# Kernel optimization log

Hardware: AMD Instinct MI355X
Metric: run time of the kernel (lower is better)

## Reference

```python
import jax, jax.numpy as jnp
import numpy as np

N, E, B = 25000, 400000, 64
IN, HID, OUT, EDGE, TDIM, L = 16, 128, 16, 16, 64, 4
EIN = 2 * HID + 1 + EDGE  # 273


def _sinusoidal(t, dim):
    half = dim // 2
    freqs = jnp.exp(jnp.arange(half, dtype=jnp.float32) * (-np.log(10000.0) / (half - 1)))
    a = t[:, None] * freqs[None, :]
    return jnp.concatenate([jnp.sin(a), jnp.cos(a)], axis=-1)


def _layernorm(h, g, b, eps=1e-5):
    mu = h.mean(-1, keepdims=True)
    v = h.var(-1, keepdims=True)
    return (h - mu) / jnp.sqrt(v + eps) * g + b


def setup_inputs() -> dict:
    key = jax.random.key(0)
    ks = iter(jax.random.split(key, 64))

    def rn(shape, scale=0.05):
        return jax.random.normal(next(ks), shape, dtype=jnp.float32) * scale

    inp = {
        'h': jax.random.normal(next(ks), (N, IN), dtype=jnp.float32),
        'x': jax.random.normal(next(ks), (N, 3), dtype=jnp.float32),
        'edge_index': jax.random.randint(next(ks), (2, E), 0, N),
        't': jax.random.uniform(next(ks), (B,), dtype=jnp.float32) * 1000.0,
        'edge_attr': jax.random.normal(next(ks), (E, EDGE), dtype=jnp.float32),
        'batch': jnp.sort(jax.random.randint(next(ks), (N,), 0, B)),
        # embeddings
        'node_w': rn((IN, HID)), 'node_b': jnp.zeros((HID,), jnp.float32),
        'tw1': rn((TDIM, HID)), 'tb1': jnp.zeros((HID,), jnp.float32),
        'tw2': rn((HID, HID)), 'tb2': jnp.zeros((HID,), jnp.float32),
        # per-layer stacked params (L, ...)
        'edge_w1': rn((L, EIN, HID)), 'edge_b1': jnp.zeros((L, HID), jnp.float32),
        'edge_w2': rn((L, HID, HID)), 'edge_b2': jnp.zeros((L, HID), jnp.float32),
        'att_w': rn((L, HID, 1)), 'att_b': jnp.zeros((L, 1), jnp.float32),
        'cw1': rn((L, HID, HID)), 'cb1': jnp.zeros((L, HID), jnp.float32),
        'cw2': rn((L, HID, 1), scale=0.001),  # xavier gain=0.001
        'nw1': rn((L, 2 * HID, HID)), 'nb1': jnp.zeros((L, HID), jnp.float32),
        'nw2': rn((L, HID, HID)), 'nb2': jnp.zeros((L, HID), jnp.float32),
        'ln_g': jnp.ones((L, HID), jnp.float32), 'ln_b': jnp.zeros((L, HID), jnp.float32),
        # heads
        'out_w1': rn((HID, HID)), 'out_b1': jnp.zeros((HID,), jnp.float32),
        'out_w2': rn((HID, OUT)), 'out_b2': jnp.zeros((OUT,), jnp.float32),
        'head_w': rn((HID, 3), scale=0.01), 'head_b': jnp.zeros((3,), jnp.float32),
    }
    return inp


def reference(h, x, edge_index, t, edge_attr, batch,
              node_w, node_b, tw1, tb1, tw2, tb2,
              edge_w1, edge_b1, edge_w2, edge_b2, att_w, att_b,
              cw1, cb1, cw2, nw1, nb1, nw2, nb2, ln_g, ln_b,
              out_w1, out_b1, out_w2, out_b2, head_w, head_b):
    silu = jax.nn.silu
    n_nodes = h.shape[0]
    row, col = edge_index[0], edge_index[1]

    # node + time embedding
    h = h @ node_w + node_b
    te = _sinusoidal(t, TDIM)
    te = silu(te @ tw1 + tb1) @ tw2 + tb2
    h = h + te[batch]

    for i in range(L):
        coord_diff = x[row] - x[col]                      # (E, 3)
        radial = (coord_diff ** 2).sum(-1, keepdims=True)  # (E, 1)
        edge_in = jnp.concatenate([h[row], h[col], radial, edge_attr], axis=-1)
        m = silu(silu(edge_in @ edge_w1[i] + edge_b1[i]) @ edge_w2[i] + edge_b2[i])
        att = jax.nn.sigmoid(m @ att_w[i] + att_b[i])
        m = m * att
        cw = silu(m @ cw1[i] + cb1[i]) @ cw2[i]           # (E, 1)
        coord_diff = coord_diff / jnp.sqrt(radial + 1e-8)  # normalize=True
        x = x + jax.ops.segment_sum(coord_diff * cw, row, num_segments=n_nodes)
        m_i = jax.ops.segment_sum(m, row, num_segments=n_nodes)
        h_in = jnp.concatenate([h, m_i], axis=-1)
        h_new = h + (silu(h_in @ nw1[i] + nb1[i]) @ nw2[i] + nb2[i])
        h = _layernorm(h_new, ln_g[i], ln_b[i])

    h_out = silu(h @ out_w1 + out_b1) @ out_w2 + out_b2  # (N, OUT)
    x_out = h @ head_w + head_b                           # (N, 3)
    return h_out, x_out
```

## Files before the change

### kernel.cpp

```cpp
#include <hip/hip_runtime.h>
#include <cmath>

#define NN      25000
#define NEDGE   400000
#define NBATCH  64
#define IN_DIM  16
#define HID     128
#define OUT_DIM 16
#define EDGE_DIM 16
#define TDIM    64
#define NL      4
#define EIN     273
#define EPB     64
#define W1KB    36
#define W2KB    16
#define A_PAD   65
#define A3OFF   (16*A_PAD*8)

typedef short bfrag __attribute__((ext_vector_type(8)));
typedef float ffrag __attribute__((ext_vector_type(4)));

__device__ __forceinline__ float siluf(float v) { return v / (1.f + __expf(-v)); }
__device__ __forceinline__ float sigm(float v)  { return 1.f / (1.f + __expf(-v)); }
__device__ __forceinline__ unsigned short f2b(float f) {
    unsigned u = __float_as_uint(f);
    u = (u + 0x7FFFu + ((u >> 16) & 1u)) >> 16;
    return (unsigned short)u;
}
__device__ __forceinline__ float b2f(unsigned short b) {
    return __uint_as_float(((unsigned)b) << 16);
}

__global__ __launch_bounds__(256) void hist_kernel(const int* __restrict__ row, int* __restrict__ deg) {
    const int tid = blockIdx.x * 256 + threadIdx.x;
    if (tid < NEDGE) atomicAdd(&deg[row[tid]], 1);
}

__global__ __launch_bounds__(1024) void scan_kernel(const int* __restrict__ deg, int* __restrict__ row_start) {
    __shared__ int part[1024];
    const int tid = threadIdx.x;
    const int base = tid * 25;
    int sum = 0;
    for (int i = 0; i < 25; i++) { const int idx = base + i; if (idx < NN) sum += deg[idx]; }
    part[tid] = sum;
    __syncthreads();
    for (int off = 1; off < 1024; off <<= 1) {
        int v = (tid >= off) ? part[tid - off] : 0;
        __syncthreads();
        part[tid] += v;
        __syncthreads();
    }
    int run = part[tid] - sum;
    for (int i = 0; i < 25; i++) {
        const int idx = base + i;
        if (idx < NN) { row_start[idx] = run; run += deg[idx]; }
    }
    if (tid == 1023) row_start[NN] = part[1023];
}

__global__ __launch_bounds__(256) void scatter_kernel(
    const int* __restrict__ row, const int* __restrict__ col,
    const int* __restrict__ row_start, int* __restrict__ cursor,
    int* __restrict__ rowp, int* __restrict__ colp, int* __restrict__ eorder)
{
    const int tid = blockIdx.x * 256 + threadIdx.x;
    if (tid >= NEDGE) return;
    const int r = row[tid];
    const int pos = row_start[r] + atomicAdd(&cursor[r], 1);
    rowp[pos] = r; colp[pos] = col[tid]; eorder[pos] = tid;
}

__global__ __launch_bounds__(256) void ea_pack(
    const float* __restrict__ ea, const int* __restrict__ eorder, unsigned short* __restrict__ eabp)
{
    const int tid = blockIdx.x * 256 + threadIdx.x;
    if (tid >= NEDGE) return;
    const int e = eorder[tid];
    const float4* src = (const float4*)&ea[(size_t)e * 16];
    bfrag o0, o1;
    #pragma unroll
    for (int q = 0; q < 2; q++) {
        const float4 a = src[q];
        o0[q*4+0] = (short)f2b(a.x); o0[q*4+1] = (short)f2b(a.y);
        o0[q*4+2] = (short)f2b(a.z); o0[q*4+3] = (short)f2b(a.w);
    }
    #pragma unroll
    for (int q = 0; q < 2; q++) {
        const float4 a = src[2+q];
        o1[q*4+0] = (short)f2b(a.x); o1[q*4+1] = (short)f2b(a.y);
        o1[q*4+2] = (short)f2b(a.z); o1[q*4+3] = (short)f2b(a.w);
    }
    *(bfrag*)&eabp[(size_t)tid * 16]     = o0;
    *(bfrag*)&eabp[(size_t)tid * 16 + 8] = o1;
}

__global__ __launch_bounds__(256) void prep_w(
    const float* __restrict__ ew1, const float* __restrict__ ew2, const float* __restrict__ cw1,
    unsigned short* __restrict__ w1p, unsigned short* __restrict__ w2p, unsigned short* __restrict__ c1p)
{
    const int PER_L = 68 * 128;
    int tid = blockIdx.x * 256 + threadIdx.x;
    if (tid >= NL * PER_L) return;
    const int l = tid / PER_L, rem = tid % PER_L;
    const int kb = rem >> 7, n = rem & 127;
    unsigned short o[8];
    if (kb < W1KB) {
        const float* W = ew1 + (size_t)l * EIN * HID;
        #pragma unroll
        for (int j = 0; j < 8; j++) {
            const int k = kb * 8 + j;
            const int ok = (k < 256) ? k : (k < 272 ? k + 1 : (k == 272 ? 256 : -1));
            o[j] = (ok >= 0) ? f2b(W[(size_t)ok * HID + n]) : (unsigned short)0;
        }
        #pragma unroll
        for (int j = 0; j < 8; j++) w1p[(((size_t)l * W1KB + kb) * 128 + n) * 8 + j] = o[j];
    } else if (kb < W1KB + W2KB) {
        const int kb2 = kb - W1KB;
        const float* W = ew2 + (size_t)l * HID * HID;
        #pragma unroll
        for (int j = 0; j < 8; j++) o[j] = f2b(W[(size_t)(kb2 * 8 + j) * HID + n]);
        #pragma unroll
        for (int j = 0; j < 8; j++) w2p[(((size_t)l * W2KB + kb2) * 128 + n) * 8 + j] = o[j];
    } else {
        const int kb2 = kb - W1KB - W2KB;
        const float* W = cw1 + (size_t)l * HID * HID;
        #pragma unroll
        for (int j = 0; j < 8; j++) o[j] = f2b(W[(size_t)(kb2 * 8 + j) * HID + n]);
        #pragma unroll
        for (int j = 0; j < 8; j++) c1p[(((size_t)l * W2KB + kb2) * 128 + n) * 8 + j] = o[j];
    }
}

__global__ __launch_bounds__(256) void prep_w2(
    const float* __restrict__ nw1, const float* __restrict__ nw2,
    const float* __restrict__ ow1, const float* __restrict__ ow2,
    unsigned short* __restrict__ n1p, unsigned short* __restrict__ n2p,
    unsigned short* __restrict__ o1p, unsigned short* __restrict__ o2p)
{
    const int C1 = NL * 32 * 128;
    const int C2 = C1 + NL * 16 * 128;
    const int C3 = C2 + 16 * 128;
    const int C4 = C3 + 16 * 16;
    int tid = blockIdx.x * 256 + threadIdx.x;
    if (tid >= C4) return;
    if (tid < C1) {
        const int l = tid / (32*128), rem = tid % (32*128);
        const int kb = rem >> 7, n = rem & 127;
        #pragma unroll
        for (int j = 0; j < 8; j++)
            n1p[(size_t)tid*8 + j] = f2b(nw1[((size_t)l*256 + kb*8 + j)*128 + n]);
    } else if (tid < C2) {
        const int t2 = tid - C1;
        const int l = t2 / (16*128), rem = t2 % (16*128);
        const int kb = rem >> 7, n = rem & 127;
        #pragma unroll
        for (int j = 0; j < 8; j++)
            n2p[(size_t)t2*8 + j] = f2b(nw2[((size_t)l*128 + kb*8 + j)*128 + n]);
    } else if (tid < C3) {
        const int t2 = tid - C2;
        const int kb = t2 >> 7, n = t2 & 127;
        #pragma unroll
        for (int j = 0; j < 8; j++)
            o1p[(size_t)t2*8 + j] = f2b(ow1[(size_t)(kb*8 + j)*128 + n]);
    } else {
        const int t2 = tid - C3;
        const int kb = t2 >> 4, n = t2 & 15;
        #pragma unroll
        for (int j = 0; j < 8; j++)
            o2p[(size_t)t2*8 + j] = f2b(ow2[(size_t)(kb*8 + j)*16 + n]);
    }
}

__global__ __launch_bounds__(HID) void te_kernel(
    const float* __restrict__ t, const float* __restrict__ tw1, const float* __restrict__ tb1,
    const float* __restrict__ tw2, const float* __restrict__ tb2, float* __restrict__ te_out)
{
    __shared__ float s0[TDIM];
    __shared__ float s1[HID];
    const int b = blockIdx.x, j = threadIdx.x;
    const float tv = t[b];
    if (j < TDIM) {
        const int k = j & 31;
        const float freq = expf((float)k * (-logf(10000.f) / 31.f));
        const float a = tv * freq;
        s0[j] = (j < 32) ? sinf(a) : cosf(a);
    }
    __syncthreads();
    float acc = tb1[j];
    for (int k = 0; k < TDIM; k++) acc += s0[k] * tw1[k*HID + j];
    s1[j] = siluf(acc);
    __syncthreads();
    float acc2 = tb2[j];
    for (int k = 0; k < HID; k++) acc2 += s1[k] * tw2[k*HID + j];
    te_out[b*HID + j] = acc2;
}

__global__ __launch_bounds__(HID) void embed_kernel(
    const float* __restrict__ h_in, const float* __restrict__ x_in,
    const int* __restrict__ batch,
    const float* __restrict__ node_w, const float* __restrict__ node_b,
    const float* __restrict__ te, float* __restrict__ h, unsigned short* __restrict__ hbf,
    float* __restrict__ x0)
{
    __shared__ float hs[IN_DIM];
    const int n = blockIdx.x, j = threadIdx.x;
    if (j < IN_DIM) hs[j] = h_in[n*IN_DIM + j];
    if (j >= 64 && j < 67) x0[n*3 + (j - 64)] = x_in[n*3 + (j - 64)];
    __syncthreads();
    float acc = node_b[j];
    #pragma unroll
    for (int k = 0; k < IN_DIM; k++) acc += hs[k] * node_w[k*HID + j];
    acc += te[batch[n]*HID + j];
    h[n*HID + j]   = acc;
    hbf[n*HID + j] = f2b(acc);
}

__global__ __launch_bounds__(256) void edge_mfma(
    const unsigned short* __restrict__ hbf, const float* __restrict__ x,
    float* __restrict__ x_new, float* __restrict__ m_i,
    const int* __restrict__ rowp, const int* __restrict__ colp,
    const unsigned short* __restrict__ eabp,
    const unsigned short* __restrict__ W1p, const float* __restrict__ B1,
    const unsigned short* __restrict__ W2p, const float* __restrict__ B2,
    const unsigned short* __restrict__ C1p, const float* __restrict__ CB1,
    const float* __restrict__ AW, const float* __restrict__ ABv,
    const float* __restrict__ CW2)
{
    __shared__ unsigned short sA[W1KB * A_PAD * 8];
    __shared__ int rc[EPB][2];
    __shared__ float AWs[HID];
    float* scr   = (float*)sA;
    float* attS  = scr;
    float* cpart = scr + 64;

    const int t = threadIdx.x;
    const int e0 = blockIdx.x * EPB;
    const int lane = t & 63, w = t >> 6;
    const int quad = lane >> 4, colid = lane & 15;

    float cd0 = 0.f, cd1 = 0.f, cd2 = 0.f;
    if (t < EPB) {
        const int r = rowp[e0 + t], c = colp[e0 + t];
        rc[t][0] = r; rc[t][1] = c;
        const float dx = x[r*3+0] - x[c*3+0];
        const float dy = x[r*3+1] - x[c*3+1];
        const float dz = x[r*3+2] - x[c*3+2];
        const float rad = dx*dx + dy*dy + dz*dz;
        const float inv = 1.f / sqrtf(rad + 1e-8f);
        cd0 = dx*inv; cd1 = dy*inv; cd2 = dz*inv;
        unsigned short* p34 = &sA[(34*A_PAD + t) * 8];
        p34[0] = f2b(rad);
        #pragma unroll
        for (int j = 1; j < 8; j++) p34[j] = 0;
        unsigned short* p35 = &sA[(35*A_PAD + t) * 8];
        #pragma unroll
        for (int j = 0; j < 8; j++) p35[j] = 0;
    }
    if (t >= 128 && t < 256) AWs[t - 128] = AW[t - 128];
    if (t < 128) {
        const int e = t >> 1, hh = t & 1;
        *(bfrag*)&sA[((32 + hh)*A_PAD + e) * 8] = *(const bfrag*)&eabp[(size_t)(e0 + e) * 16 + hh * 8];
    }
    __syncthreads();
    #pragma unroll
    for (int it = 0; it < 8; it++) {
        const int c = t + it * 256;
        const int e = (c >> 4) & 63;
        const int half = c >> 10;
        const int kb16 = c & 15;
        const int node = rc[e][half];
        *(bfrag*)&sA[((half*16 + kb16)*A_PAD + e) * 8] = *(const bfrag*)&hbf[(size_t)node * HID + kb16 * 8];
    }
    __syncthreads();

    ffrag acc1[4][2] = {};
    for (int ks = 0; ks < 9; ks++) {
        const int kb = ks * 4 + quad;
        const bfrag b0 = *(const bfrag*)&W1p[((size_t)kb * 128 + w*32 + colid) * 8];
        const bfrag b1 = *(const bfrag*)&W1p[((size_t)kb * 128 + w*32 + 16 + colid) * 8];
        #pragma unroll
        for (int mt = 0; mt < 4; mt++) {
            const bfrag a = *(const bfrag*)&sA[(kb*A_PAD + mt*16 + colid) * 8];
            acc1[mt][0] = __builtin_amdgcn_mfma_f32_16x16x32_bf16(a, b0, acc1[mt][0], 0, 0, 0);
            acc1[mt][1] = __builtin_amdgcn_mfma_f32_16x16x32_bf16(a, b1, acc1[mt][1], 0, 0, 0);
        }
    }
    __syncthreads();
    {
        const float bias0 = B1[w*32 + colid], bias1 = B1[w*32 + 16 + colid];
        #pragma unroll
        for (int mt = 0; mt < 4; mt++)
            #pragma unroll
            for (int nt = 0; nt < 2; nt++) {
                const float bb = nt ? bias1 : bias0;
                const int f = w*32 + nt*16 + colid;
                const int kb = f >> 3, j = f & 7;
                #pragma unroll
                for (int reg = 0; reg < 4; reg++) {
                    const float v = siluf(acc1[mt][nt][reg] + bb);
                    const int e = mt*16 + quad*4 + reg;
                    sA[(kb*A_PAD + e) * 8 + j] = f2b(v);
                }
            }
    }
    __syncthreads();

    ffrag acc2[4][2] = {};
    for (int ks = 0; ks < 4; ks++) {
        const int kb = ks * 4 + quad;
        const bfrag b0 = *(const bfrag*)&W2p[((size_t)kb * 128 + w*32 + colid) * 8];
        const bfrag b1 = *(const bfrag*)&W2p[((size_t)kb * 128 + w*32 + 16 + colid) * 8];
        #pragma unroll
        for (int mt = 0; mt < 4; mt++) {
            const bfrag a = *(const bfrag*)&sA[(kb*A_PAD + mt*16 + colid) * 8];
            acc2[mt][0] = __builtin_amdgcn_mfma_f32_16x16x32_bf16(a, b0, acc2[mt][0], 0, 0, 0);
            acc2[mt][1] = __builtin_amdgcn_mfma_f32_16x16x32_bf16(a, b1, acc2[mt][1], 0, 0, 0);
        }
    }
    {
        const float bias0 = B2[w*32 + colid], bias1 = B2[w*32 + 16 + colid];
        #pragma unroll
        for (int mt = 0; mt < 4; mt++)
            #pragma unroll
            for (int nt = 0; nt < 2; nt++) {
                const float bb = nt ? bias1 : bias0;
                const int f = w*32 + nt*16 + colid;
                const int kb = f >> 3, j = f & 7;
                #pragma unroll
                for (int reg = 0; reg < 4; reg++) {
                    const float v = siluf(acc2[mt][nt][reg] + bb);
                    const int e = mt*16 + quad*4 + reg;
                    sA[A3OFF + (kb*A_PAD + e) * 8 + j] = f2b(v);
                }
            }
    }
    __syncthreads();

    {
        const int e = t >> 2, q = t & 3;
        float s = 0.f;
        #pragma unroll
        for (int kk = 0; kk < 4; kk++) {
            const int kb = q*4 + kk;
            const bfrag v = *(const bfrag*)&sA[A3OFF + (kb*A_PAD + e) * 8];
            #pragma unroll
            for (int j = 0; j < 8; j++) s += b2f((unsigned short)v[j]) * AWs[kb*8 + j];
        }
        s += __shfl_xor(s, 1);
        s += __shfl_xor(s, 2);
        if (q == 0) attS[e] = sigm(s + ABv[0]);
    }
    __syncthreads();

    {
        const int f0 = lane, f1 = lane + 64;
        float a0 = 0.f, a1 = 0.f;
        for (int i = 0; i < 16; i++) {
            const int e = (w << 4) + i;
            const float av = attS[e];
            const int r = rc[e][0];
            const int idx0 = A3OFF + ((f0 >> 3)*A_PAD + e) * 8 + (f0 & 7);
            const float v0 = b2f(sA[idx0]) * av;
            sA[idx0] = f2b(v0); a0 += v0;
            const int idx1 = A3OFF + ((f1 >> 3)*A_PAD + e) * 8 + (f1 & 7);
            const float v1 = b2f(sA[idx1]) * av;
            sA[idx1] = f2b(v1); a1 += v1;
            const bool flush = (i == 15) || (rc[e+1][0] != r);
            if (flush) {
                atomicAdd(&m_i[(size_t)r * HID + f0], a0);
                atomicAdd(&m_i[(size_t)r * HID + f1], a1);
                a0 = 0.f; a1 = 0.f;
            }
        }
    }
    __syncthreads();

    ffrag acc3[4][2] = {};
    for (int ks = 0; ks < 4; ks++) {
        const int kb = ks * 4 + quad;
        const bfrag b0 = *(const bfrag*)&C1p[((size_t)kb * 128 + w*32 + colid) * 8];
        const bfrag b1 = *(const bfrag*)&C1p[((size_t)kb * 128 + w*32 + 16 + colid) * 8];
        #pragma unroll
        for (int mt = 0; mt < 4; mt++) {
            const bfrag a = *(const bfrag*)&sA[A3OFF + (kb*A_PAD + mt*16 + colid) * 8];
            acc3[mt][0] = __builtin_amdgcn_mfma_f32_16x16x32_bf16(a, b0, acc3[mt][0], 0, 0, 0);
            acc3[mt][1] = __builtin_amdgcn_mfma_f32_16x16x32_bf16(a, b1, acc3[mt][1], 0, 0, 0);
        }
    }
    {
        const float cb0v = CB1[w*32 + colid], cb1v = CB1[w*32 + 16 + colid];
        const float cwv0 = CW2[w*32 + colid], cwv1 = CW2[w*32 + 16 + colid];
        float p[4][4];
        #pragma unroll
        for (int mt = 0; mt < 4; mt++)
            #pragma unroll
            for (int reg = 0; reg < 4; reg++) p[mt][reg] = 0.f;
        #pragma unroll
        for (int mt = 0; mt < 4; mt++)
            #pragma unroll
            for (int nt = 0; nt < 2; nt++) {
                const float cb = nt ? cb1v : cb0v;
                const float cw = nt ? cwv1 : cwv0;
                #pragma unroll
                for (int reg = 0; reg < 4; reg++)
                    p[mt][reg] += siluf(acc3[mt][nt][reg] + cb) * cw;
            }
        #pragma unroll
        for (int mt = 0; mt < 4; mt++)
            #pragma unroll
            for (int reg = 0; reg < 4; reg++) {
                float s = p[mt][reg];
                s += __shfl_xor(s, 1);
                s += __shfl_xor(s, 2);
                s += __shfl_xor(s, 4);
                s += __shfl_xor(s, 8);
                if (colid == 0) cpart[(mt*16 + quad*4 + reg) * 4 + w] = s;
            }
    }
    __syncthreads();
    if (t < EPB) {
        const float s = cpart[t*4+0] + cpart[t*4+1] + cpart[t*4+2] + cpart[t*4+3];
        const int r = rc[t][0];
        atomicAdd(&x_new[r*3+0], cd0 * s);
        atomicAdd(&x_new[r*3+1], cd1 * s);
        atomicAdd(&x_new[r*3+2], cd2 * s);
    }
}

__global__ __launch_bounds__(256) void node_mfma(
    float* __restrict__ h, unsigned short* __restrict__ hbf, const float* __restrict__ m_i,
    const unsigned short* __restrict__ N1p, const float* __restrict__ NB1,
    const unsigned short* __restrict__ N2p, const float* __restrict__ NB2,
    const float* __restrict__ LG, const float* __restrict__ LB)
{
    __shared__ unsigned short sA[32 * A_PAD * 8];
    __shared__ float mu_s[64], rs_s[64];
    float* hres = (float*)sA;

    const int t = threadIdx.x, lane = t & 63, w = t >> 6;
    const int quad = lane >> 4, colid = lane & 15;
    const int n0 = blockIdx.x * 64;

    #pragma unroll
    for (int it = 0; it < 4; it++) {
        const int c = t + it * 256;
        const int e = c >> 4, kb = c & 15;
        const int nidx = min(n0 + e, NN - 1);
        *(bfrag*)&sA[(kb*A_PAD + e) * 8] = *(const bfrag*)&hbf[(size_t)nidx * HID + kb * 8];
    }
    #pragma unroll
    for (int it = 0; it < 4; it++) {
        const int c = t + it * 256;
        const int e = c >> 4, kb = c & 15;
        const int nidx = min(n0 + e, NN - 1);
        const float4 v0 = *(const float4*)&m_i[(size_t)nidx * HID + kb * 8];
        const float4 v1 = *(const float4*)&m_i[(size_t)nidx * HID + kb * 8 + 4];
        bfrag bv;
        bv[0]=(short)f2b(v0.x); bv[1]=(short)f2b(v0.y); bv[2]=(short)f2b(v0.z); bv[3]=(short)f2b(v0.w);
        bv[4]=(short)f2b(v1.x); bv[5]=(short)f2b(v1.y); bv[6]=(short)f2b(v1.z); bv[7]=(short)f2b(v1.w);
        *(bfrag*)&sA[((16 + kb)*A_PAD + e) * 8] = bv;
    }
    __syncthreads();

    ffrag acc1[4][2] = {};
    for (int ks = 0; ks < 8; ks++) {
        const int kb = ks * 4 + quad;
        const bfrag b0 = *(const bfrag*)&N1p[((size_t)kb * 128 + w*32 + colid) * 8];
        const bfrag b1 = *(const bfrag*)&N1p[((size_t)kb * 128 + w*32 + 16 + colid) * 8];
        #pragma unroll
        for (int mt = 0; mt < 4; mt++) {
            const bfrag a = *(const bfrag*)&sA[(kb*A_PAD + mt*16 + colid) * 8];
            acc1[mt][0] = __builtin_amdgcn_mfma_f32_16x16x32_bf16(a, b0, acc1[mt][0], 0, 0, 0);
            acc1[mt][1] = __builtin_amdgcn_mfma_f32_16x16x32_bf16(a, b1, acc1[mt][1], 0, 0, 0);
        }
    }
    __syncthreads();
    {
        const float bias0 = NB1[w*32 + colid], bias1 = NB1[w*32 + 16 + colid];
        #pragma unroll
        for (int mt = 0; mt < 4; mt++)
            #pragma unroll
            for (int nt = 0; nt < 2; nt++) {
                const float bb = nt ? bias1 : bias0;
                const int f = w*32 + nt*16 + colid;
                const int kb = f >> 3, j = f & 7;
                #pragma unroll
                for (int reg = 0; reg < 4; reg++) {
                    const float v = siluf(acc1[mt][nt][reg] + bb);
                    const int e = mt*16 + quad*4 + reg;
                    sA[(kb*A_PAD + e) * 8 + j] = f2b(v);
                }
            }
    }
    __syncthreads();

    ffrag acc2[4][2] = {};
    for (int ks = 0; ks < 4; ks++) {
        const int kb = ks * 4 + quad;
        const bfrag b0 = *(const bfrag*)&N2p[((size_t)kb * 128 + w*32 + colid) * 8];
        const bfrag b1 = *(const bfrag*)&N2p[((size_t)kb * 128 + w*32 + 16 + colid) * 8];
        #pragma unroll
        for (int mt = 0; mt < 4; mt++) {
            const bfrag a = *(const bfrag*)&sA[(kb*A_PAD + mt*16 + colid) * 8];
            acc2[mt][0] = __builtin_amdgcn_mfma_f32_16x16x32_bf16(a, b0, acc2[mt][0], 0, 0, 0);
            acc2[mt][1] = __builtin_amdgcn_mfma_f32_16x16x32_bf16(a, b1, acc2[mt][1], 0, 0, 0);
        }
    }
    __syncthreads();
    {
        const float bias0 = NB2[w*32 + colid], bias1 = NB2[w*32 + 16 + colid];
        #pragma unroll
        for (int mt = 0; mt < 4; mt++)
            #pragma unroll
            for (int nt = 0; nt < 2; nt++) {
                const float bb = nt ? bias1 : bias0;
                const int f = w*32 + nt*16 + colid;
                #pragma unroll
                for (int reg = 0; reg < 4; reg++) {
                    const int row = mt*16 + quad*4 + reg;
                    const int nidx = min(n0 + row, NN - 1);
                    hres[row*129 + f] = acc2[mt][nt][reg] + bb + h[(size_t)nidx*HID + f];
                }
            }
    }
    __syncthreads();
    {
        const int row = t >> 2, q = t & 3;
        float s = 0.f, s2 = 0.f;
        #pragma unroll
        for (int i = 0; i < 32; i++) {
            const float v = hres[row*129 + q*32 + i];
            s += v; s2 += v*v;
        }
        s += __shfl_xor(s, 1); s2 += __shfl_xor(s2, 1);
        s += __shfl_xor(s, 2); s2 += __shfl_xor(s2, 2);
        if (q == 0) {
            const float mu = s * (1.f/HID);
            mu_s[row] = mu;
            rs_s[row] = rsqrtf(s2 * (1.f/HID) - mu*mu + 1e-5f);
        }
    }
    __syncthreads();
    for (int idx = t; idx < 64*HID; idx += 256) {
        const int row = idx >> 7, f = idx & 127;
        const int n = n0 + row;
        if (n < NN) {
            const float v = (hres[row*129 + f] - mu_s[row]) * rs_s[row] * LG[f] + LB[f];
            h[(size_t)n*HID + f]   = v;
            hbf[(size_t)n*HID + f] = f2b(v);
        }
    }
}

__global__ __launch_bounds__(256) void out_mfma(
    const unsigned short* __restrict__ hbf,
    const unsigned short* __restrict__ O1p, const float* __restrict__ OB1,
    const unsigned short* __restrict__ O2p, const float* __restrict__ OB2,
    const float* __restrict__ HW, const float* __restrict__ HB,
    float* __restrict__ out)
{
    __shared__ unsigned short sA[32 * A_PAD * 8];
    __shared__ float hws[HID*3];
    const int A2O = 16 * A_PAD * 8;

    const int t = threadIdx.x, lane = t & 63, w = t >> 6;
    const int quad = lane >> 4, colid = lane & 15;
    const int n0 = blockIdx.x * 64;

    if (t < 128)      { hws[t] = HW[t]; hws[t+128] = HW[t+128]; }
    else if (t < 256) { const int i = t - 128 + 256; if (i < 384) hws[i] = HW[i]; }
    #pragma unroll
    for (int it = 0; it < 4; it++) {
        const int c = t + it * 256;
        const int e = c >> 4, kb = c & 15;
        const int nidx = min(n0 + e, NN - 1);
        *(bfrag*)&sA[(kb*A_PAD + e) * 8] = *(const bfrag*)&hbf[(size_t)nidx * HID + kb * 8];
    }
    __syncthreads();

    ffrag acc1[4][2] = {};
    for (int ks = 0; ks < 4; ks++) {
        const int kb = ks * 4 + quad;
        const bfrag b0 = *(const bfrag*)&O1p[((size_t)kb * 128 + w*32 + colid) * 8];
        const bfrag b1 = *(const bfrag*)&O1p[((size_t)kb * 128 + w*32 + 16 + colid) * 8];
        #pragma unroll
        for (int mt = 0; mt < 4; mt++) {
            const bfrag a = *(const bfrag*)&sA[(kb*A_PAD + mt*16 + colid) * 8];
            acc1[mt][0] = __builtin_amdgcn_mfma_f32_16x16x32_bf16(a, b0, acc1[mt][0], 0, 0, 0);
            acc1[mt][1] = __builtin_amdgcn_mfma_f32_16x16x32_bf16(a, b1, acc1[mt][1], 0, 0, 0);
        }
    }
    {
        const float bias0 = OB1[w*32 + colid], bias1 = OB1[w*32 + 16 + colid];
        #pragma unroll
        for (int mt = 0; mt < 4; mt++)
            #pragma unroll
            for (int nt = 0; nt < 2; nt++) {
                const float bb = nt ? bias1 : bias0;
                const int f = w*32 + nt*16 + colid;
                const int kb = f >> 3, j = f & 7;
                #pragma unroll
                for (int reg = 0; reg < 4; reg++) {
                    const float v = siluf(acc1[mt][nt][reg] + bb);
                    const int e = mt*16 + quad*4 + reg;
                    sA[A2O + (kb*A_PAD + e) * 8 + j] = f2b(v);
                }
            }
    }
    __syncthreads();

    ffrag acco = {};
    for (int ks = 0; ks < 4; ks++) {
        const int kb = ks * 4 + quad;
        const bfrag a = *(const bfrag*)&sA[A2O + (kb*A_PAD + w*16 + colid) * 8];
        const bfrag b = *(const bfrag*)&O2p[((size_t)kb * 16 + colid) * 8];
        acco = __builtin_amdgcn_mfma_f32_16x16x32_bf16(a, b, acco, 0, 0, 0);
    }
    #pragma unroll
    for (int reg = 0; reg < 4; reg++) {
        const int rowg = w*16 + quad*4 + reg;
        const int n = n0 + rowg;
        if (n < NN) out[(size_t)n*OUT_DIM + colid] = acco[reg] + OB2[colid];
    }

    {
        const int rloc = t >> 2, q = t & 3;
        float s0 = 0.f, s1 = 0.f, s2 = 0.f;
        #pragma unroll
        for (int kk = 0; kk < 4; kk++) {
            const int kb = q*4 + kk;
            const bfrag v = *(const bfrag*)&sA[(kb*A_PAD + rloc) * 8];
            #pragma unroll
            for (int j = 0; j < 8; j++) {
                const float hv = b2f((unsigned short)v[j]);
                const int k = kb*8 + j;
                s0 += hv * hws[k*3+0]; s1 += hv * hws[k*3+1]; s2 += hv * hws[k*3+2];
            }
        }
        s0 += __shfl_xor(s0, 1); s1 += __shfl_xor(s1, 1); s2 += __shfl_xor(s2, 1);
        s0 += __shfl_xor(s0, 2); s1 += __shfl_xor(s1, 2); s2 += __shfl_xor(s2, 2);
        const int n = n0 + rloc;
        if (q == 0 && n < NN) {
            out[(size_t)NN*OUT_DIM + n*3 + 0] = s0 + HB[0];
            out[(size_t)NN*OUT_DIM + n*3 + 1] = s1 + HB[1];
            out[(size_t)NN*OUT_DIM + n*3 + 2] = s2 + HB[2];
        }
    }
}

extern "C" void kernel_launch(void* const* d_in, const int* in_sizes, int n_in,
                              void* d_out, int out_size, void* d_ws, size_t ws_size,
                              hipStream_t stream) {
    (void)in_sizes; (void)n_in; (void)out_size; (void)ws_size;
    const float* h_in      = (const float*)d_in[0];
    const float* x_in      = (const float*)d_in[1];
    const int*   edge_idx  = (const int*)  d_in[2];
    const float* t         = (const float*)d_in[3];
    const float* edge_attr = (const float*)d_in[4];
    const int*   batch     = (const int*)  d_in[5];
    const float* node_w = (const float*)d_in[6];
    const float* node_b = (const float*)d_in[7];
    const float* tw1    = (const float*)d_in[8];
    const float* tb1    = (const float*)d_in[9];
    const float* tw2    = (const float*)d_in[10];
    const float* tb2    = (const float*)d_in[11];
    const float* ew1    = (const float*)d_in[12];
    const float* eb1    = (const float*)d_in[13];
    const float* ew2    = (const float*)d_in[14];
    const float* eb2    = (const float*)d_in[15];
    const float* attw   = (const float*)d_in[16];
    const float* attb   = (const float*)d_in[17];
    const float* cw1    = (const float*)d_in[18];
    const float* cb1    = (const float*)d_in[19];
    const float* cw2    = (const float*)d_in[20];
    const float* nw1    = (const float*)d_in[21];
    const float* nb1    = (const float*)d_in[22];
    const float* nw2    = (const float*)d_in[23];
    const float* nb2    = (const float*)d_in[24];
    const float* lng    = (const float*)d_in[25];
    const float* lnb    = (const float*)d_in[26];
    const float* ow1    = (const float*)d_in[27];
    const float* ob1    = (const float*)d_in[28];
    const float* ow2    = (const float*)d_in[29];
    const float* ob2    = (const float*)d_in[30];
    const float* hw     = (const float*)d_in[31];
    const float* hb     = (const float*)d_in[32];

    const int* row = edge_idx;
    const int* col = edge_idx + NEDGE;

    float* ws  = (float*)d_ws;
    float* te  = ws;
    float* h   = te  + NBATCH*HID;
    float* m_i = h   + (size_t)NN*HID;
    float* x0  = m_i + (size_t)NN*HID;
    float* x1  = x0  + NN*3;
    unsigned short* hbf  = (unsigned short*)(x1 + NN*3);
    unsigned short* eabp = hbf + (size_t)NN*HID;
    unsigned short* w1p  = eabp + (size_t)NEDGE*EDGE_DIM;
    unsigned short* w2p  = w1p + (size_t)NL*W1KB*128*8;
    unsigned short* c1p  = w2p + (size_t)NL*W2KB*128*8;
    unsigned short* n1p  = c1p + (size_t)NL*W2KB*128*8;
    unsigned short* n2p  = n1p + (size_t)NL*32*128*8;
    unsigned short* o1p  = n2p + (size_t)NL*16*128*8;
    unsigned short* o2p  = o1p + (size_t)16*128*8;
    int* deg       = (int*)(o2p + 16*16*8);
    int* row_start = deg + NN;
    int* cursor    = row_start + NN + 1;
    int* rowp      = cursor + NN;
    int* colp      = rowp + NEDGE;
    int* eorder    = colp + NEDGE;

    hipMemsetAsync(deg, 0, NN*sizeof(int), stream);
    hipMemsetAsync(cursor, 0, NN*sizeof(int), stream);
    hist_kernel<<<(NEDGE+255)/256, 256, 0, stream>>>(row, deg);
    scan_kernel<<<1, 1024, 0, stream>>>(deg, row_start);
    scatter_kernel<<<(NEDGE+255)/256, 256, 0, stream>>>(row, col, row_start, cursor, rowp, colp, eorder);
    ea_pack<<<(NEDGE+255)/256, 256, 0, stream>>>(edge_attr, eorder, eabp);

    prep_w<<<(NL*68*128 + 255)/256, 256, 0, stream>>>(ew1, ew2, cw1, w1p, w2p, c1p);
    prep_w2<<<(NL*32*128 + NL*16*128 + 16*128 + 16*16 + 255)/256, 256, 0, stream>>>(
        nw1, nw2, ow1, ow2, n1p, n2p, o1p, o2p);
    te_kernel<<<NBATCH, HID, 0, stream>>>(t, tw1, tb1, tw2, tb2, te);
    embed_kernel<<<NN, HID, 0, stream>>>(h_in, x_in, batch, node_w, node_b, te, h, hbf, x0);

    const int NBLK = (NN + 63) / 64;
    float* xc = x0; float* xn = x1;
    for (int i = 0; i < NL; i++) {
        hipMemsetAsync(m_i, 0, (size_t)NN*HID*sizeof(float), stream);
        hipMemcpyAsync(xn, xc, (size_t)NN*3*sizeof(float), hipMemcpyDeviceToDevice, stream);
        edge_mfma<<<NEDGE/EPB, 256, 0, stream>>>(
            hbf, xc, xn, m_i, rowp, colp, eabp,
            w1p + (size_t)i*W1KB*128*8, eb1 + (size_t)i*HID,
            w2p + (size_t)i*W2KB*128*8, eb2 + (size_t)i*HID,
            c1p + (size_t)i*W2KB*128*8, cb1 + (size_t)i*HID,
            attw + (size_t)i*HID, attb + i,
            cw2 + (size_t)i*HID);
        node_mfma<<<NBLK, 256, 0, stream>>>(
            h, hbf, m_i,
            n1p + (size_t)i*32*128*8, nb1 + (size_t)i*HID,
            n2p + (size_t)i*16*128*8, nb2 + (size_t)i*HID,
            lng + (size_t)i*HID,      lnb + (size_t)i*HID);
        float* tmp = xc; xc = xn; xn = tmp;
    }

    out_mfma<<<NBLK, 256, 0, stream>>>(hbf, o1p, ob1, o2p, ob2, hw, hb, (float*)d_out);
}
```

Measured before the change: 1.193 ms.

## Fold attention scale into coord MLP epilogue and pack bf16 LDS stores

The per-edge attention scale is no longer written back into shared memory before the coordinate MLP. The C1 matmul now runs on the unscaled activations and the scale is applied to its accumulator in the epilogue, using the linearity of the matmul. This removes one barrier and a read-modify-write pass over the tile. The segment-sum loop now reads two packed bf16 values per lane, and the SiLU epilogues swap values between paired lanes so each lane writes one bf16x2 instead of scalar shorts. A barrier is added before cpart is written, because cpart aliases the shared buffer that the scatter loop still reads.

```diff
diff --git a/kernel.cpp b/kernel.cpp
--- a/kernel.cpp
+++ b/kernel.cpp
@@ -1,4 +1,5 @@
 #include <hip/hip_runtime.h>
+#include <hip/hip_bf16.h>
 #include <cmath>
 
 #define NN      25000
@@ -237,6 +238,7 @@
     const int e0 = blockIdx.x * EPB;
     const int lane = t & 63, w = t >> 6;
     const int quad = lane >> 4, colid = lane & 15;
+    const int pl = lane & 1;
 
     float cd0 = 0.f, cd1 = 0.f, cd2 = 0.f;
     if (t < EPB) {
@@ -287,19 +289,28 @@
     }
     __syncthreads();
     {
+        const int kbw = w*4 + (colid >> 3);
+        const int j0  = colid & 6;
         const float bias0 = B1[w*32 + colid], bias1 = B1[w*32 + 16 + colid];
         #pragma unroll
         for (int mt = 0; mt < 4; mt++)
             #pragma unroll
             for (int nt = 0; nt < 2; nt++) {
                 const float bb = nt ? bias1 : bias0;
-                const int f = w*32 + nt*16 + colid;
-                const int kb = f >> 3, j = f & 7;
-                #pragma unroll
-                for (int reg = 0; reg < 4; reg++) {
-                    const float v = siluf(acc1[mt][nt][reg] + bb);
+                float v[4], p[4];
+                #pragma unroll
+                for (int reg = 0; reg < 4; reg++) v[reg] = siluf(acc1[mt][nt][reg] + bb);
+                #pragma unroll
+                for (int reg = 0; reg < 4; reg++) p[reg] = __shfl_xor(v[reg], 1);
+                const int kb = kbw + nt*2;
+                #pragma unroll
+                for (int rr = 0; rr < 2; rr++) {
+                    const int reg = rr*2 + pl;
                     const int e = mt*16 + quad*4 + reg;
-                    sA[(kb*A_PAD + e) * 8 + j] = f2b(v);
+                    const float lo = pl ? p[reg] : v[reg];
+                    const float hi = pl ? v[reg] : p[reg];
+                    *(__hip_bfloat162*)&sA[(kb*A_PAD + e) * 8 + j0] =
+                        __float22bfloat162_rn(make_float2(lo, hi));
                 }
             }
     }
@@ -318,19 +329,28 @@
         }
     }
     {
+        const int kbw = w*4 + (colid >> 3);
+        const int j0  = colid & 6;
         const float bias0 = B2[w*32 + colid], bias1 = B2[w*32 + 16 + colid];
         #pragma unroll
         for (int mt = 0; mt < 4; mt++)
             #pragma unroll
             for (int nt = 0; nt < 2; nt++) {
                 const float bb = nt ? bias1 : bias0;
-                const int f = w*32 + nt*16 + colid;
-                const int kb = f >> 3, j = f & 7;
-                #pragma unroll
-                for (int reg = 0; reg < 4; reg++) {
-                    const float v = siluf(acc2[mt][nt][reg] + bb);
+                float v[4], p[4];
+                #pragma unroll
+                for (int reg = 0; reg < 4; reg++) v[reg] = siluf(acc2[mt][nt][reg] + bb);
+                #pragma unroll
+                for (int reg = 0; reg < 4; reg++) p[reg] = __shfl_xor(v[reg], 1);
+                const int kb = kbw + nt*2;
+                #pragma unroll
+                for (int rr = 0; rr < 2; rr++) {
+                    const int reg = rr*2 + pl;
                     const int e = mt*16 + quad*4 + reg;
-                    sA[A3OFF + (kb*A_PAD + e) * 8 + j] = f2b(v);
+                    const float lo = pl ? p[reg] : v[reg];
+                    const float hi = pl ? v[reg] : p[reg];
+                    *(__hip_bfloat162*)&sA[A3OFF + (kb*A_PAD + e) * 8 + j0] =
+                        __float22bfloat162_rn(make_float2(lo, hi));
                 }
             }
     }
@@ -352,44 +372,49 @@
     }
     __syncthreads();
 
-    {
-        const int f0 = lane, f1 = lane + 64;
+    ffrag acc3[4][2] = {};
+    for (int ks = 0; ks < 4; ks++) {
+        const int kb = ks * 4 + quad;
+        const bfrag b0 = *(const bfrag*)&C1p[((size_t)kb * 128 + w*32 + colid) * 8];
+        const bfrag b1 = *(const bfrag*)&C1p[((size_t)kb * 128 + w*32 + 16 + colid) * 8];
+        #pragma unroll
+        for (int mt = 0; mt < 4; mt++) {
+            const bfrag a = *(const bfrag*)&sA[A3OFF + (kb*A_PAD + mt*16 + colid) * 8];
+            acc3[mt][0] = __builtin_amdgcn_mfma_f32_16x16x32_bf16(a, b0, acc3[mt][0], 0, 0, 0);
+            acc3[mt][1] = __builtin_amdgcn_mfma_f32_16x16x32_bf16(a, b1, acc3[mt][1], 0, 0, 0);
+        }
+    }
+
+    {
+        const int fkb = lane >> 2;
+        const int fj  = (lane & 3) * 2;
+        const int fcol = 2 * lane;
         float a0 = 0.f, a1 = 0.f;
         for (int i = 0; i < 16; i++) {
             const int e = (w << 4) + i;
             const float av = attS[e];
             const int r = rc[e][0];
-            const int idx0 = A3OFF + ((f0 >> 3)*A_PAD + e) * 8 + (f0 & 7);
-            const float v0 = b2f(sA[idx0]) * av;
-            sA[idx0] = f2b(v0); a0 += v0;
-            const int idx1 = A3OFF + ((f1 >> 3)*A_PAD + e) * 8 + (f1 & 7);
-            const float v1 = b2f(sA[idx1]) * av;
-            sA[idx1] = f2b(v1); a1 += v1;
+            const unsigned v32 = *(const unsigned*)&sA[A3OFF + (fkb*A_PAD + e) * 8 + fj];
+            a0 += __uint_as_float(v32 << 16) * av;
+            a1 += __uint_as_float(v32 & 0xFFFF0000u) * av;
             const bool flush = (i == 15) || (rc[e+1][0] != r);
             if (flush) {
-                atomicAdd(&m_i[(size_t)r * HID + f0], a0);
-                atomicAdd(&m_i[(size_t)r * HID + f1], a1);
+                atomicAdd(&m_i[(size_t)r * HID + fcol],     a0);
+                atomicAdd(&m_i[(size_t)r * HID + fcol + 1], a1);
                 a0 = 0.f; a1 = 0.f;
             }
         }
     }
-    __syncthreads();
-
-    ffrag acc3[4][2] = {};
-    for (int ks = 0; ks < 4; ks++) {
-        const int kb = ks * 4 + quad;
-        const bfrag b0 = *(const bfrag*)&C1p[((size_t)kb * 128 + w*32 + colid) * 8];
-        const bfrag b1 = *(const bfrag*)&C1p[((size_t)kb * 128 + w*32 + 16 + colid) * 8];
-        #pragma unroll
-        for (int mt = 0; mt < 4; mt++) {
-            const bfrag a = *(const bfrag*)&sA[A3OFF + (kb*A_PAD + mt*16 + colid) * 8];
-            acc3[mt][0] = __builtin_amdgcn_mfma_f32_16x16x32_bf16(a, b0, acc3[mt][0], 0, 0, 0);
-            acc3[mt][1] = __builtin_amdgcn_mfma_f32_16x16x32_bf16(a, b1, acc3[mt][1], 0, 0, 0);
-        }
-    }
+
     {
         const float cb0v = CB1[w*32 + colid], cb1v = CB1[w*32 + 16 + colid];
         const float cwv0 = CW2[w*32 + colid], cwv1 = CW2[w*32 + 16 + colid];
+        float att_r[4][4];
+        #pragma unroll
+        for (int mt = 0; mt < 4; mt++) {
+            const float4 a4 = *(const float4*)&attS[mt*16 + quad*4];
+            att_r[mt][0] = a4.x; att_r[mt][1] = a4.y; att_r[mt][2] = a4.z; att_r[mt][3] = a4.w;
+        }
         float p[4][4];
         #pragma unroll
         for (int mt = 0; mt < 4; mt++)
@@ -403,8 +428,9 @@
                 const float cw = nt ? cwv1 : cwv0;
                 #pragma unroll
                 for (int reg = 0; reg < 4; reg++)
-                    p[mt][reg] += siluf(acc3[mt][nt][reg] + cb) * cw;
-            }
+                    p[mt][reg] += siluf(att_r[mt][reg] * acc3[mt][nt][reg] + cb) * cw;
+            }
+        __syncthreads();
         #pragma unroll
         for (int mt = 0; mt < 4; mt++)
             #pragma unroll
```

Result: slower. 1.474 ms (+23.5%).
